# Optimization experiments

Measured on AMD Instinct MI355X. Metric: run time of the kernel, lower is better.

The kernel has to match this reference:

```python
import jax, jax.numpy as jnp
import numpy as np
import math

B, S, D = 8, 1024, 512      # batch, seq_len, d_model
H = 8                       # n_heads
DK = D                      # per-head dim forced to d_model by the view() quirk
EPS = 1e-6


def setup_inputs() -> dict:
    key = jax.random.key(0)
    ks = jax.random.split(key, 8)
    # xavier_uniform for (out, in) = (H*DK, D)
    lim_qkv = math.sqrt(6.0 / (H * DK + D))
    lim_fc = math.sqrt(6.0 / (D + H * DK))
    return {
        "q": jax.random.normal(ks[0], (B, S, D), jnp.float32),
        "k": jax.random.normal(ks[1], (B, S, D), jnp.float32),
        "v": jax.random.normal(ks[2], (B, S, D), jnp.float32),
        "w_q": jax.random.uniform(ks[3], (H * DK, D), jnp.float32, -lim_qkv, lim_qkv),
        "w_k": jax.random.uniform(ks[4], (H * DK, D), jnp.float32, -lim_qkv, lim_qkv),
        "w_v": jax.random.uniform(ks[5], (H * DK, D), jnp.float32, -lim_qkv, lim_qkv),
        "w_fc": jax.random.uniform(ks[6], (D, H * DK), jnp.float32, -lim_fc, lim_fc),
        "gamma": jnp.ones((D,), jnp.float32),
        "beta": jnp.zeros((D,), jnp.float32),
    }


def reference(q, k, v, w_q, w_k, w_v, w_fc, gamma, beta):
    residual = q
    # project then view as (B, S, H, d_q) with d_q = d_model (source's quirk)
    qh = (q @ w_q.T).reshape(B, S, H, DK).transpose(0, 2, 1, 3)  # (B,H,S,DK)
    kh = (k @ w_k.T).reshape(B, S, H, DK).transpose(0, 2, 1, 3)
    vh = (v @ w_v.T).reshape(B, S, H, DK).transpose(0, 2, 1, 3)
    # scaled dot-product attention; scale by sqrt(d_q) = sqrt(d_model)
    scale = 1.0 / math.sqrt(DK)
    attn = jnp.einsum("bhqd,bhkd->bhqk", qh, kh) * scale  # (B,H,S,S)
    attn = jax.nn.softmax(attn, axis=-1)
    out = jnp.einsum("bhqk,bhkd->bhqd", attn, vh)          # (B,H,S,DK)
    out = out.transpose(0, 2, 1, 3).reshape(B, S, H * DK)  # (B,S,H*DK)
    out = out @ w_fc.T                                      # (B,S,D); dropout = identity (eval)
    out = out + residual
    # LayerNorm(eps=1e-6)
    mu = jnp.mean(out, axis=-1, keepdims=True)
    var = jnp.var(out, axis=-1, keepdims=True)
    out = (out - mu) * jax.lax.rsqrt(var + EPS) * gamma + beta
    return out
```

## Files before the change

kernel.cpp:

```cpp
#include <hip/hip_runtime.h>
#include <hip/hip_bf16.h>
#include <stdint.h>

typedef __attribute__((ext_vector_type(8))) short short8;
typedef __attribute__((ext_vector_type(4))) float f32x4;

__device__ __forceinline__ short f2bf(float f) {
  __hip_bfloat16 h = __float2bfloat16(f);
  union { __hip_bfloat16 h; short s; } x;
  x.h = h;
  return x.s;
}
__device__ __forceinline__ void g2lds16(const void* g, void* l) {
  __builtin_amdgcn_global_load_lds(
      (const __attribute__((address_space(1))) void*)g,
      (__attribute__((address_space(3))) void*)l, 16, 0, 0);
}

__global__ void cvt6(const float* __restrict__ q, const float* __restrict__ k,
                     const float* __restrict__ v, const float* __restrict__ wq,
                     const float* __restrict__ wk, const float* __restrict__ wv,
                     short* __restrict__ xb, short* __restrict__ wb)
{
  const int z = blockIdx.z;
  const float* s;
  short* d;
  long nvec;
  if (z < 3) { s = (z == 0) ? q : (z == 1) ? k : v;  d = xb + (long)z * 4194304; nvec = 524288; }
  else       { s = (z == 3) ? wq : (z == 4) ? wk : wv; d = wb + (long)(z - 3) * 2097152; nvec = 262144; }
  const long stride = (long)gridDim.x * blockDim.x;
  for (long i = (long)blockIdx.x * blockDim.x + threadIdx.x; i < nvec; i += stride) {
    f32x4 a = *(const f32x4*)(s + i * 8);
    f32x4 b = *(const f32x4*)(s + i * 8 + 4);
    short8 o;
#pragma unroll
    for (int t = 0; t < 4; ++t) { o[t] = f2bf(a[t]); o[4 + t] = f2bf(b[t]); }
    *(short8*)(d + i * 8) = o;
  }
}

__global__ void cvt1(const float* __restrict__ s, short* __restrict__ d, int nvec)
{
  const long stride = (long)gridDim.x * blockDim.x;
  for (long i = (long)blockIdx.x * blockDim.x + threadIdx.x; i < nvec; i += stride) {
    f32x4 a = *(const f32x4*)(s + i * 8);
    f32x4 b = *(const f32x4*)(s + i * 8 + 4);
    short8 o;
#pragma unroll
    for (int t = 0; t < 4; ++t) { o[t] = f2bf(a[t]); o[4 + t] = f2bf(b[t]); }
    *(short8*)(d + i * 8) = o;
  }
}

__global__ void qkv_proj(
    const short* __restrict__ xb, const short* __restrict__ wb,
    short* __restrict__ Qh, short* __restrict__ Kh, short* __restrict__ Vt)
{
  __shared__ __align__(16) short As[128 * 32];
  __shared__ __align__(16) short Bs[128 * 32];
  const int z = blockIdx.z;
  const short* x = xb + (long)z * 4194304;
  const short* W = wb + (long)z * 2097152;
  short* out = (z == 0) ? Qh : (z == 1) ? Kh : Vt;
  const int tid = threadIdx.x;
  const int wave = tid >> 6, lane = tid & 63;
  const int quad = lane >> 4, l15 = lane & 15;
  const int mBase = blockIdx.x * 128, nBase = blockIdx.y * 128;
  const int wm = wave >> 1, wn = wave & 1;
  const int c0 = tid, c1 = tid + 256;
  const int r0 = c0 >> 2, o0 = (c0 & 3) * 8;
  const int r1 = c1 >> 2, o1 = (c1 & 3) * 8;
  f32x4 acc[4][4] = {};

  for (int k0 = 0; k0 < 512; k0 += 32) {
    __syncthreads();
    g2lds16(x + (long)(mBase + r0) * 512 + k0 + o0, (char*)As + c0 * 16);
    g2lds16(x + (long)(mBase + r1) * 512 + k0 + o1, (char*)As + c1 * 16);
    g2lds16(W + (long)(nBase + r0) * 512 + k0 + o0, (char*)Bs + c0 * 16);
    g2lds16(W + (long)(nBase + r1) * 512 + k0 + o1, (char*)Bs + c1 * 16);
    __syncthreads();
    short8 a[4], b[4];
#pragma unroll
    for (int mi = 0; mi < 4; ++mi)
      a[mi] = *(const short8*)(As + (wm * 64 + mi * 16 + l15) * 32 + quad * 8);
#pragma unroll
    for (int ni = 0; ni < 4; ++ni)
      b[ni] = *(const short8*)(Bs + (wn * 64 + ni * 16 + l15) * 32 + quad * 8);
#pragma unroll
    for (int mi = 0; mi < 4; ++mi)
#pragma unroll
      for (int ni = 0; ni < 4; ++ni)
        acc[mi][ni] = __builtin_amdgcn_mfma_f32_16x16x32_bf16(a[mi], b[ni], acc[mi][ni], 0, 0, 0);
  }
#pragma unroll
  for (int mi = 0; mi < 4; ++mi) {
#pragma unroll
    for (int ni = 0; ni < 4; ++ni) {
      int n = nBase + wn * 64 + ni * 16 + l15;
      int h = n >> 9, d = n & 511;
#pragma unroll
      for (int r = 0; r < 4; ++r) {
        int m = mBase + wm * 64 + mi * 16 + quad * 4 + r;
        int b = m >> 10, s = m & 1023;
        long idx;
        if (z == 2) idx = ((long)(b * 8 + h) * 512 + d) * 1024 + s;
        else        idx = ((long)(b * 8 + h) * 1024 + s) * 512 + d;
        out[idx] = f2bf(acc[mi][ni][r]);
      }
    }
  }
}

__global__ __launch_bounds__(256, 2) void flash_attn(
    const short* __restrict__ Qh, const short* __restrict__ Kh,
    const short* __restrict__ Vt, short* __restrict__ ctx)
{
  __shared__ __align__(16) short Ks[32 * 512];
  __shared__ __align__(16) short Vs[512 * 32];
  __shared__ __align__(16) short Ps[4 * 16 * 40];
  __shared__ float lred[64];
  const int tid = threadIdx.x;
  const int wave = tid >> 6, lane = tid & 63;
  const int quad = lane >> 4, l15 = lane & 15;
  const int lin = blockIdx.x;
  const int qt = (lin >> 3) & 15;
  const int bh = ((lin >> 7) << 3) | (lin & 7);
  const float C = 0.0637587234f;

  const short* qbase = Qh + ((long)bh * 1024 + qt * 64 + wave * 16 + l15) * 512 + quad * 8;
  short8 qf[16];
#pragma unroll
  for (int c = 0; c < 16; ++c) qf[c] = *(const short8*)(qbase + c * 32);

  f32x4 acc[4][8] = {};
  float l[4] = {0.f, 0.f, 0.f, 0.f};

  for (int kt = 0; kt < 32; ++kt) {
    __syncthreads();
#pragma unroll
    for (int i = 0; i < 8; ++i) {
      int c = i * 256 + tid;
      int r = c >> 6, j = (c & 63) ^ (r & 7);
      g2lds16(Kh + ((long)bh * 1024 + kt * 32 + r) * 512 + j * 8, (char*)Ks + c * 16);
    }
    __builtin_amdgcn_sched_barrier(0);
#pragma unroll
    for (int i = 0; i < 8; ++i) {
      int c = i * 256 + tid;
      int d = c >> 2, j = (c & 3) ^ (d & 3);
      g2lds16(Vt + ((long)bh * 512 + d) * 1024 + kt * 32 + j * 8, (char*)Vs + c * 16);
    }
    __builtin_amdgcn_sched_barrier(0);
    asm volatile("s_waitcnt vmcnt(8)" ::: "memory");
    __builtin_amdgcn_s_barrier();
    __builtin_amdgcn_sched_barrier(0);

    f32x4 sacc[2] = {};
#pragma unroll
    for (int nt = 0; nt < 2; ++nt)
#pragma unroll
      for (int c = 0; c < 16; ++c) {
        int row = nt * 16 + l15;
        int j = (c * 4 + quad) ^ (row & 7);
        short8 kf = *(const short8*)(Ks + row * 512 + j * 8);
        sacc[nt] = __builtin_amdgcn_mfma_f32_16x16x32_bf16(qf[c], kf, sacc[nt], 0, 0, 0);
      }
#pragma unroll
    for (int r = 0; r < 4; ++r) {
      float p0 = exp2f(sacc[0][r] * C);
      float p1 = exp2f(sacc[1][r] * C);
      Ps[wave * 640 + (quad * 4 + r) * 40 + l15]      = f2bf(p0);
      Ps[wave * 640 + (quad * 4 + r) * 40 + 16 + l15] = f2bf(p1);
      l[r] += p0 + p1;
    }
    __syncthreads();

    short8 vf[8];
#pragma unroll
    for (int t = 0; t < 8; ++t) {
      int row = wave * 128 + t * 16 + l15;
      int j = quad ^ (row & 3);
      vf[t] = *(const short8*)(Vs + row * 32 + j * 8);
    }
#pragma unroll
    for (int g = 0; g < 4; ++g) {
      short8 pf = *(const short8*)(Ps + g * 640 + l15 * 40 + quad * 8);
#pragma unroll
      for (int t = 0; t < 8; ++t)
        acc[g][t] = __builtin_amdgcn_mfma_f32_16x16x32_bf16(pf, vf[t], acc[g][t], 0, 0, 0);
    }
  }
#pragma unroll
  for (int r = 0; r < 4; ++r) {
    float t = l[r];
    t += __shfl_xor(t, 1);
    t += __shfl_xor(t, 2);
    t += __shfl_xor(t, 4);
    t += __shfl_xor(t, 8);
    l[r] = t;
  }
  if (l15 == 0) {
#pragma unroll
    for (int r = 0; r < 4; ++r) lred[wave * 16 + quad * 4 + r] = l[r];
  }
  __syncthreads();
  const int b = bh >> 3, h = bh & 7;
#pragma unroll
  for (int g = 0; g < 4; ++g) {
#pragma unroll
    for (int r = 0; r < 4; ++r) {
      float inv = 1.0f / lred[g * 16 + quad * 4 + r];
      int qrow = qt * 64 + g * 16 + quad * 4 + r;
      long base = ((long)(b * 1024 + qrow)) * 4096 + h * 512 + wave * 128;
#pragma unroll
      for (int t = 0; t < 8; ++t)
        ctx[base + t * 16 + l15] = f2bf(acc[g][t][r] * inv);
    }
  }
}

__global__ void fc_gemm(
    const short* __restrict__ A, const short* __restrict__ Wb,
    const float* __restrict__ resid, float* __restrict__ Y)
{
  __shared__ __align__(16) short As[128 * 32];
  __shared__ __align__(16) short Bs[64 * 32];
  const int tid = threadIdx.x;
  const int wave = tid >> 6, lane = tid & 63;
  const int quad = lane >> 4, l15 = lane & 15;
  const int mBase = blockIdx.x * 128, nBase = blockIdx.y * 64;
  const int wm = wave >> 1, wn = wave & 1;
  const int c0 = tid, c1 = tid + 256;
  const int r0 = c0 >> 2, o0 = (c0 & 3) * 8;
  const int r1 = c1 >> 2, o1 = (c1 & 3) * 8;
  f32x4 acc[4][2] = {};

  for (int k0 = 0; k0 < 4096; k0 += 32) {
    __syncthreads();
    g2lds16(A + (long)(mBase + r0) * 4096 + k0 + o0, (char*)As + c0 * 16);
    g2lds16(A + (long)(mBase + r1) * 4096 + k0 + o1, (char*)As + c1 * 16);
    g2lds16(Wb + (long)(nBase + r0) * 4096 + k0 + o0, (char*)Bs + c0 * 16);
    __syncthreads();
    short8 a[4], b[2];
#pragma unroll
    for (int mi = 0; mi < 4; ++mi)
      a[mi] = *(const short8*)(As + (wm * 64 + mi * 16 + l15) * 32 + quad * 8);
#pragma unroll
    for (int ni = 0; ni < 2; ++ni)
      b[ni] = *(const short8*)(Bs + (wn * 32 + ni * 16 + l15) * 32 + quad * 8);
#pragma unroll
    for (int mi = 0; mi < 4; ++mi)
#pragma unroll
      for (int ni = 0; ni < 2; ++ni)
        acc[mi][ni] = __builtin_amdgcn_mfma_f32_16x16x32_bf16(a[mi], b[ni], acc[mi][ni], 0, 0, 0);
  }
#pragma unroll
  for (int mi = 0; mi < 4; ++mi)
#pragma unroll
    for (int ni = 0; ni < 2; ++ni) {
      int n = nBase + wn * 32 + ni * 16 + l15;
#pragma unroll
      for (int r = 0; r < 4; ++r) {
        int m = mBase + wm * 64 + mi * 16 + quad * 4 + r;
        long idx = (long)m * 512 + n;
        Y[idx] = acc[mi][ni][r] + resid[idx];
      }
    }
}

__global__ void layernorm(
    const float* __restrict__ Y, const float* __restrict__ gamma,
    const float* __restrict__ beta, float* __restrict__ out)
{
  const int tid = threadIdx.x;
  const int wave = tid >> 6, lane = tid & 63;
  const long row = (long)blockIdx.x * 4 + wave;
  f32x4 xa = *(const f32x4*)(Y + row * 512 + lane * 8);
  f32x4 xb = *(const f32x4*)(Y + row * 512 + lane * 8 + 4);
  float x[8];
  float s = 0.f, s2 = 0.f;
#pragma unroll
  for (int i = 0; i < 4; ++i) { x[i] = xa[i]; x[i + 4] = xb[i]; }
#pragma unroll
  for (int i = 0; i < 8; ++i) { s += x[i]; s2 += x[i] * x[i]; }
#pragma unroll
  for (int m = 1; m < 64; m <<= 1) { s += __shfl_xor(s, m); s2 += __shfl_xor(s2, m); }
  float mu = s * (1.0f / 512.0f);
  float var = s2 * (1.0f / 512.0f) - mu * mu;
  float rs = rsqrtf(var + 1e-6f);
  f32x4 oa, ob;
#pragma unroll
  for (int i = 0; i < 4; ++i) {
    oa[i] = (x[i] - mu) * rs * gamma[lane * 8 + i] + beta[lane * 8 + i];
    ob[i] = (x[i + 4] - mu) * rs * gamma[lane * 8 + 4 + i] + beta[lane * 8 + 4 + i];
  }
  *(f32x4*)(out + row * 512 + lane * 8) = oa;
  *(f32x4*)(out + row * 512 + lane * 8 + 4) = ob;
}

extern "C" void kernel_launch(void* const* d_in, const int* in_sizes, int n_in,
                              void* d_out, int out_size, void* d_ws, size_t ws_size,
                              hipStream_t stream) {
  const float* q     = (const float*)d_in[0];
  const float* k     = (const float*)d_in[1];
  const float* v     = (const float*)d_in[2];
  const float* wq    = (const float*)d_in[3];
  const float* wk    = (const float*)d_in[4];
  const float* wv    = (const float*)d_in[5];
  const float* wfc   = (const float*)d_in[6];
  const float* gamma = (const float*)d_in[7];
  const float* beta  = (const float*)d_in[8];
  float* out = (float*)d_out;
  char* ws = (char*)d_ws;
  short* Qh  = (short*)(ws);
  short* Kh  = (short*)(ws + 67108864);
  short* Vt  = (short*)(ws + 134217728);
  short* ctx = (short*)(ws + 201326592);
  short* xb  = (short*)(ws + 201326592);
  short* wb  = xb + 3 * 4194304;
  short* wfcb = (short*)(ws + 16777216);
  float* Y   = (float*)(ws);

  cvt6<<<dim3(1024, 1, 6), 256, 0, stream>>>(q, k, v, wq, wk, wv, xb, wb);
  qkv_proj<<<dim3(64, 32, 3), 256, 0, stream>>>(xb, wb, Qh, Kh, Vt);
  flash_attn<<<dim3(1024), 256, 0, stream>>>(Qh, Kh, Vt, ctx);
  cvt1<<<dim3(1024), 256, 0, stream>>>(wfc, wfcb, 262144);
  fc_gemm<<<dim3(64, 8), 256, 0, stream>>>(ctx, wfcb, q, Y);
  layernorm<<<2048, 256, 0, stream>>>(Y, gamma, beta, out);
}
```

Before: 717.9 us.

## Double-buffer LDS tiles in projection, attention and output GEMM kernels

Adds ping-pong LDS buffers to qkv_proj, flash_attn and fc_gemm. The next K-tile is prefetched with global_load_lds while the current one is consumed, using partial vmcnt waits and raw s_barriers in place of two __syncthreads per iteration. The aim is to hide global load latency behind MFMA work. Flash attention now needs 128KB of LDS, so its launch bounds drop to one block per SM, which lowers occupancy. The last iteration also issues a redundant wrap-around prefetch.

```diff
diff --git a/kernel.cpp b/kernel.cpp
--- a/kernel.cpp
+++ b/kernel.cpp
@@ -56,8 +56,8 @@
     const short* __restrict__ xb, const short* __restrict__ wb,
     short* __restrict__ Qh, short* __restrict__ Kh, short* __restrict__ Vt)
 {
-  __shared__ __align__(16) short As[128 * 32];
-  __shared__ __align__(16) short Bs[128 * 32];
+  __shared__ __align__(16) short As[2][128 * 32];
+  __shared__ __align__(16) short Bs[2][128 * 32];
   const int z = blockIdx.z;
   const short* x = xb + (long)z * 4194304;
   const short* W = wb + (long)z * 2097152;
@@ -72,26 +72,38 @@
   const int r1 = c1 >> 2, o1 = (c1 & 3) * 8;
   f32x4 acc[4][4] = {};
 
-  for (int k0 = 0; k0 < 512; k0 += 32) {
-    __syncthreads();
-    g2lds16(x + (long)(mBase + r0) * 512 + k0 + o0, (char*)As + c0 * 16);
-    g2lds16(x + (long)(mBase + r1) * 512 + k0 + o1, (char*)As + c1 * 16);
-    g2lds16(W + (long)(nBase + r0) * 512 + k0 + o0, (char*)Bs + c0 * 16);
-    g2lds16(W + (long)(nBase + r1) * 512 + k0 + o1, (char*)Bs + c1 * 16);
-    __syncthreads();
+  auto stage = [&](int kk, int b_) {
+    g2lds16(x + (long)(mBase + r0) * 512 + kk + o0, (char*)(As[b_]) + c0 * 16);
+    g2lds16(x + (long)(mBase + r1) * 512 + kk + o1, (char*)(As[b_]) + c1 * 16);
+    g2lds16(W + (long)(nBase + r0) * 512 + kk + o0, (char*)(Bs[b_]) + c0 * 16);
+    g2lds16(W + (long)(nBase + r1) * 512 + kk + o1, (char*)(Bs[b_]) + c1 * 16);
+  };
+  stage(0, 0);
+
+  for (int it = 0; it < 16; ++it) {
+    const int buf = it & 1;
+    stage(((it + 1) & 15) * 32, buf ^ 1);
+    __builtin_amdgcn_sched_barrier(0);
+    asm volatile("s_waitcnt vmcnt(4)" ::: "memory");
+    __builtin_amdgcn_s_barrier();
+    __builtin_amdgcn_sched_barrier(0);
     short8 a[4], b[4];
 #pragma unroll
     for (int mi = 0; mi < 4; ++mi)
-      a[mi] = *(const short8*)(As + (wm * 64 + mi * 16 + l15) * 32 + quad * 8);
+      a[mi] = *(const short8*)(As[buf] + (wm * 64 + mi * 16 + l15) * 32 + quad * 8);
 #pragma unroll
     for (int ni = 0; ni < 4; ++ni)
-      b[ni] = *(const short8*)(Bs + (wn * 64 + ni * 16 + l15) * 32 + quad * 8);
+      b[ni] = *(const short8*)(Bs[buf] + (wn * 64 + ni * 16 + l15) * 32 + quad * 8);
 #pragma unroll
     for (int mi = 0; mi < 4; ++mi)
 #pragma unroll
       for (int ni = 0; ni < 4; ++ni)
         acc[mi][ni] = __builtin_amdgcn_mfma_f32_16x16x32_bf16(a[mi], b[ni], acc[mi][ni], 0, 0, 0);
-  }
+    __builtin_amdgcn_s_barrier();
+    __builtin_amdgcn_sched_barrier(0);
+  }
+  asm volatile("s_waitcnt vmcnt(0)" ::: "memory");
+
 #pragma unroll
   for (int mi = 0; mi < 4; ++mi) {
 #pragma unroll
@@ -111,12 +123,12 @@
   }
 }
 
-__global__ __launch_bounds__(256, 2) void flash_attn(
+__global__ __launch_bounds__(256, 1) void flash_attn(
     const short* __restrict__ Qh, const short* __restrict__ Kh,
     const short* __restrict__ Vt, short* __restrict__ ctx)
 {
-  __shared__ __align__(16) short Ks[32 * 512];
-  __shared__ __align__(16) short Vs[512 * 32];
+  __shared__ __align__(16) short Ks[2][32 * 512];
+  __shared__ __align__(16) short Vs[2][512 * 32];
   __shared__ __align__(16) short Ps[4 * 16 * 40];
   __shared__ float lred[64];
   const int tid = threadIdx.x;
@@ -132,29 +144,34 @@
 #pragma unroll
   for (int c = 0; c < 16; ++c) qf[c] = *(const short8*)(qbase + c * 32);
 
-  f32x4 acc[4][8] = {};
-  float l[4] = {0.f, 0.f, 0.f, 0.f};
-
-  for (int kt = 0; kt < 32; ++kt) {
-    __syncthreads();
+  auto stage = [&](int kt_, int b_) {
 #pragma unroll
     for (int i = 0; i < 8; ++i) {
       int c = i * 256 + tid;
       int r = c >> 6, j = (c & 63) ^ (r & 7);
-      g2lds16(Kh + ((long)bh * 1024 + kt * 32 + r) * 512 + j * 8, (char*)Ks + c * 16);
-    }
-    __builtin_amdgcn_sched_barrier(0);
+      g2lds16(Kh + ((long)bh * 1024 + kt_ * 32 + r) * 512 + j * 8, (char*)(Ks[b_]) + c * 16);
+    }
 #pragma unroll
     for (int i = 0; i < 8; ++i) {
       int c = i * 256 + tid;
       int d = c >> 2, j = (c & 3) ^ (d & 3);
-      g2lds16(Vt + ((long)bh * 512 + d) * 1024 + kt * 32 + j * 8, (char*)Vs + c * 16);
-    }
-    __builtin_amdgcn_sched_barrier(0);
-    asm volatile("s_waitcnt vmcnt(8)" ::: "memory");
-    __builtin_amdgcn_s_barrier();
-    __builtin_amdgcn_sched_barrier(0);
-
+      g2lds16(Vt + ((long)bh * 512 + d) * 1024 + kt_ * 32 + j * 8, (char*)(Vs[b_]) + c * 16);
+    }
+  };
+  stage(0, 0);
+
+  f32x4 acc[4][8] = {};
+  float l[4] = {0.f, 0.f, 0.f, 0.f};
+
+  for (int kt = 0; kt < 32; ++kt) {
+    const int buf = kt & 1;
+    stage((kt + 1) & 31, buf ^ 1);
+    __builtin_amdgcn_sched_barrier(0);
+    asm volatile("s_waitcnt vmcnt(16)" ::: "memory");
+    __builtin_amdgcn_s_barrier();
+    __builtin_amdgcn_sched_barrier(0);
+
+    const short* ks = Ks[buf];
     f32x4 sacc[2] = {};
 #pragma unroll
     for (int nt = 0; nt < 2; ++nt)
@@ -162,7 +179,7 @@
       for (int c = 0; c < 16; ++c) {
         int row = nt * 16 + l15;
         int j = (c * 4 + quad) ^ (row & 7);
-        short8 kf = *(const short8*)(Ks + row * 512 + j * 8);
+        short8 kf = *(const short8*)(ks + row * 512 + j * 8);
         sacc[nt] = __builtin_amdgcn_mfma_f32_16x16x32_bf16(qf[c], kf, sacc[nt], 0, 0, 0);
       }
 #pragma unroll
@@ -173,14 +190,17 @@
       Ps[wave * 640 + (quad * 4 + r) * 40 + 16 + l15] = f2bf(p1);
       l[r] += p0 + p1;
     }
-    __syncthreads();
-
+    asm volatile("s_waitcnt lgkmcnt(0)" ::: "memory");
+    __builtin_amdgcn_s_barrier();
+    __builtin_amdgcn_sched_barrier(0);
+
+    const short* vs = Vs[buf];
     short8 vf[8];
 #pragma unroll
     for (int t = 0; t < 8; ++t) {
       int row = wave * 128 + t * 16 + l15;
       int j = quad ^ (row & 3);
-      vf[t] = *(const short8*)(Vs + row * 32 + j * 8);
+      vf[t] = *(const short8*)(vs + row * 32 + j * 8);
     }
 #pragma unroll
     for (int g = 0; g < 4; ++g) {
@@ -189,6 +209,8 @@
       for (int t = 0; t < 8; ++t)
         acc[g][t] = __builtin_amdgcn_mfma_f32_16x16x32_bf16(pf, vf[t], acc[g][t], 0, 0, 0);
     }
+    __builtin_amdgcn_s_barrier();
+    __builtin_amdgcn_sched_barrier(0);
   }
 #pragma unroll
   for (int r = 0; r < 4; ++r) {
@@ -223,8 +245,8 @@
     const short* __restrict__ A, const short* __restrict__ Wb,
     const float* __restrict__ resid, float* __restrict__ Y)
 {
-  __shared__ __align__(16) short As[128 * 32];
-  __shared__ __align__(16) short Bs[64 * 32];
+  __shared__ __align__(16) short As[2][128 * 32];
+  __shared__ __align__(16) short Bs[2][64 * 32];
   const int tid = threadIdx.x;
   const int wave = tid >> 6, lane = tid & 63;
   const int quad = lane >> 4, l15 = lane & 15;
@@ -235,25 +257,37 @@
   const int r1 = c1 >> 2, o1 = (c1 & 3) * 8;
   f32x4 acc[4][2] = {};
 
-  for (int k0 = 0; k0 < 4096; k0 += 32) {
-    __syncthreads();
-    g2lds16(A + (long)(mBase + r0) * 4096 + k0 + o0, (char*)As + c0 * 16);
-    g2lds16(A + (long)(mBase + r1) * 4096 + k0 + o1, (char*)As + c1 * 16);
-    g2lds16(Wb + (long)(nBase + r0) * 4096 + k0 + o0, (char*)Bs + c0 * 16);
-    __syncthreads();
+  auto stage = [&](int kk, int b_) {
+    g2lds16(A + (long)(mBase + r0) * 4096 + kk + o0, (char*)(As[b_]) + c0 * 16);
+    g2lds16(A + (long)(mBase + r1) * 4096 + kk + o1, (char*)(As[b_]) + c1 * 16);
+    g2lds16(Wb + (long)(nBase + r0) * 4096 + kk + o0, (char*)(Bs[b_]) + c0 * 16);
+  };
+  stage(0, 0);
+
+  for (int it = 0; it < 128; ++it) {
+    const int buf = it & 1;
+    stage(((it + 1) & 127) * 32, buf ^ 1);
+    __builtin_amdgcn_sched_barrier(0);
+    asm volatile("s_waitcnt vmcnt(3)" ::: "memory");
+    __builtin_amdgcn_s_barrier();
+    __builtin_amdgcn_sched_barrier(0);
     short8 a[4], b[2];
 #pragma unroll
     for (int mi = 0; mi < 4; ++mi)
-      a[mi] = *(const short8*)(As + (wm * 64 + mi * 16 + l15) * 32 + quad * 8);
+      a[mi] = *(const short8*)(As[buf] + (wm * 64 + mi * 16 + l15) * 32 + quad * 8);
 #pragma unroll
     for (int ni = 0; ni < 2; ++ni)
-      b[ni] = *(const short8*)(Bs + (wn * 32 + ni * 16 + l15) * 32 + quad * 8);
+      b[ni] = *(const short8*)(Bs[buf] + (wn * 32 + ni * 16 + l15) * 32 + quad * 8);
 #pragma unroll
     for (int mi = 0; mi < 4; ++mi)
 #pragma unroll
       for (int ni = 0; ni < 2; ++ni)
         acc[mi][ni] = __builtin_amdgcn_mfma_f32_16x16x32_bf16(a[mi], b[ni], acc[mi][ni], 0, 0, 0);
-  }
+    __builtin_amdgcn_s_barrier();
+    __builtin_amdgcn_sched_barrier(0);
+  }
+  asm volatile("s_waitcnt vmcnt(0)" ::: "memory");
+
 #pragma unroll
   for (int mi = 0; mi < 4; ++mi)
 #pragma unroll
```

After: 729.6 us. No clear change (+1.6%).
